# Performance work log

Hardware: AMD Instinct MI355X
Metric: run time of the kernel (lower is better)

## Reference

```python
import jax, jax.numpy as jnp
import numpy as np

D_MODEL = 512
D_INNER = 1024           # expand=2 * d_model
HEADDIM = 1024           # headdim = 2*hidden_dim -> nheads = 1
NHEADS = 1
D_STATE = 128            # Mamba2 default
D_CONV = 4               # Mamba2 default
CONV_DIM = D_INNER + 2 * D_STATE   # 1280
D_IN_PROJ = 2 * D_INNER + 2 * D_STATE + NHEADS  # 2305
BATCH, SEQ = 8, 2048
EPS = 1e-5


def setup_inputs() -> dict:
    key = jax.random.key(0)
    ks = jax.random.split(key, 8)
    x = jax.random.normal(ks[0], (BATCH, SEQ, D_MODEL), dtype=jnp.float32)
    rnn_state = jnp.zeros((1, BATCH, D_MODEL), dtype=jnp.float32)
    W_in = jax.random.normal(ks[1], (D_MODEL, D_IN_PROJ), dtype=jnp.float32) * 0.02
    conv_w = jax.random.normal(ks[2], (CONV_DIM, D_CONV), dtype=jnp.float32) * 0.2
    conv_b = jnp.zeros((CONV_DIM,), dtype=jnp.float32)
    dt_bias = jax.random.normal(ks[3], (NHEADS,), dtype=jnp.float32) * 0.1
    # A in (-16, -1): A_log = log(uniform(1,16))
    A_log = jnp.log(jax.random.uniform(ks[4], (NHEADS,), minval=1.0, maxval=16.0, dtype=jnp.float32))
    D = jnp.ones((NHEADS,), dtype=jnp.float32)
    norm_w = jnp.ones((D_INNER,), dtype=jnp.float32)
    W_out = jax.random.normal(ks[5], (D_INNER, D_MODEL), dtype=jnp.float32) * 0.02
    return {"x": x, "rnn_state": rnn_state, "W_in": W_in, "conv_w": conv_w,
            "conv_b": conv_b, "dt_bias": dt_bias, "A_log": A_log, "D": D,
            "norm_w": norm_w, "W_out": W_out}


def _mamba2_forward(x, W_in, conv_w, conv_b, dt_bias, A_log, D, norm_w, W_out):
    Bsz, T, _ = x.shape
    zxbcdt = x @ W_in                              # [B,T,2305]
    z = zxbcdt[..., :D_INNER]                      # [B,T,1024]
    xBC = zxbcdt[..., D_INNER:D_INNER + CONV_DIM]  # [B,T,1280]
    dt = zxbcdt[..., -NHEADS:]                     # [B,T,1]

    # causal depthwise conv1d over time, then silu
    xBC_t = jnp.transpose(xBC, (0, 2, 1))          # [B,C,T]
    w = conv_w[:, None, :]                          # [C,1,K]
    conv = jax.lax.conv_general_dilated(
        xBC_t, w, window_strides=(1,), padding=[(D_CONV - 1, 0)],
        feature_group_count=CONV_DIM, dimension_numbers=("NCH", "OIH", "NCH"))
    xBC = jax.nn.silu(jnp.transpose(conv, (0, 2, 1)) + conv_b)  # [B,T,1280]

    x_ssm = xBC[..., :D_INNER].reshape(Bsz, T, NHEADS, HEADDIM)  # [B,T,H,P]
    Bm = xBC[..., D_INNER:D_INNER + D_STATE]       # [B,T,N] (ngroups=1)
    Cm = xBC[..., -D_STATE:]                       # [B,T,N]

    dt = jax.nn.softplus(dt + dt_bias)             # [B,T,H]
    A = -jnp.exp(A_log)                            # [H]

    # selective SSM recurrence over time (time-major scan)
    xs = (jnp.transpose(x_ssm, (1, 0, 2, 3)),      # [T,B,H,P]
          jnp.transpose(dt, (1, 0, 2)),            # [T,B,H]
          jnp.transpose(Bm, (1, 0, 2)),            # [T,B,N]
          jnp.transpose(Cm, (1, 0, 2)))            # [T,B,N]
    h0 = jnp.zeros((Bsz, NHEADS, HEADDIM, D_STATE), dtype=x.dtype)

    def step(h, inp):
        xt, dtt, Bt, Ct = inp
        dA = jnp.exp(dtt * A)                      # [B,H]
        h = h * dA[:, :, None, None] + (dtt[:, :, None] * xt)[..., None] * Bt[:, None, None, :]
        y = jnp.einsum("bhpn,bn->bhp", h, Ct)
        return h, y

    _, ys = jax.lax.scan(step, h0, xs)             # ys: [T,B,H,P]
    y = jnp.transpose(ys, (1, 0, 2, 3)) + x_ssm * D[None, None, :, None]
    y = y.reshape(Bsz, T, D_INNER)

    # gated RMSNorm (norm_before_gate=False): rmsnorm(y * silu(z)) * weight
    y = y * jax.nn.silu(z)
    y = y * jax.lax.rsqrt(jnp.mean(y * y, axis=-1, keepdims=True) + EPS) * norm_w
    return y @ W_out                               # [B,T,D_MODEL]


def reference(x, rnn_state, W_in, conv_w, conv_b, dt_bias, A_log, D, norm_w, W_out):
    out = _mamba2_forward(x, W_in, conv_w, conv_b, dt_bias, A_log, D, norm_w, W_out)
    return (out, rnn_state)
```

## Files before the change

### kernel.cpp

```cpp
#include <hip/hip_runtime.h>
#include <hip/hip_bf16.h>
#include <math.h>

#define D_MODEL 512
#define D_INNER 1024
#define D_STATE 128
#define CONV_DIM (D_INNER + 2*D_STATE)
#define D_IN_PROJ (2*D_INNER + 2*D_STATE + 1)
#define NPROJ 2304
#define BATCH 8
#define SEQ 2048
#define NROWS (BATCH*SEQ)
#define CHUNK 128
#define NCHUNK (NROWS/CHUNK)
#define CPB (SEQ/CHUNK)
#define EPS_RMS 1e-5f

typedef __hip_bfloat16 bf16;
typedef __attribute__((ext_vector_type(8))) short short8;
typedef __attribute__((ext_vector_type(4))) float f32x4;

__device__ __forceinline__ float fbf(bf16 v) { return __bfloat162float(v); }
__device__ __forceinline__ bf16 tbf(float v) { return __float2bfloat16(v); }

__device__ __forceinline__ void gl2lds16(const bf16* g, bf16* l) {
    __builtin_amdgcn_global_load_lds(
        (const __attribute__((address_space(1))) unsigned int*)g,
        (__attribute__((address_space(3))) unsigned int*)l, 16, 0, 0);
}

__global__ void k_transpose_cvt(const float* __restrict__ src, bf16* __restrict__ dst,
                                int R, int C, int sstride) {
    __shared__ float tile[32][33];
    int c0 = blockIdx.x * 32, r0 = blockIdx.y * 32;
    int tx = threadIdx.x, ty = threadIdx.y;
    #pragma unroll
    for (int i = 0; i < 32; i += 8)
        tile[ty + i][tx] = src[(size_t)(c0 + ty + i) * sstride + (r0 + tx)];
    __syncthreads();
    #pragma unroll
    for (int i = 0; i < 32; i += 8)
        dst[(size_t)(r0 + ty + i) * C + (c0 + tx)] = tbf(tile[tx][ty + i]);
}

__global__ __launch_bounds__(256) void k_dtcvt(
    const float* __restrict__ x, const float* __restrict__ W_in,
    const float* __restrict__ dt_bias,
    bf16* __restrict__ xb, float* __restrict__ dts)
{
    __shared__ float wcol[D_MODEL];
    int tid = threadIdx.x;
    wcol[tid]       = W_in[(size_t)tid * D_IN_PROJ + 2304];
    wcol[tid + 256] = W_in[(size_t)(tid + 256) * D_IN_PROJ + 2304];
    __syncthreads();
    int row  = blockIdx.x * 4 + (tid >> 6);
    int lane = tid & 63;
    const float* xr = x + (size_t)row * D_MODEL;
    float4 a = *(const float4*)(xr + lane * 8);
    float4 b = *(const float4*)(xr + lane * 8 + 4);
    union { bf16 o[8]; uint4 u; } pk;
    pk.o[0]=tbf(a.x); pk.o[1]=tbf(a.y); pk.o[2]=tbf(a.z); pk.o[3]=tbf(a.w);
    pk.o[4]=tbf(b.x); pk.o[5]=tbf(b.y); pk.o[6]=tbf(b.z); pk.o[7]=tbf(b.w);
    *(uint4*)(xb + (size_t)row * D_MODEL + lane * 8) = pk.u;
    const float* wc = wcol + lane * 8;
    float s = a.x*wc[0]+a.y*wc[1]+a.z*wc[2]+a.w*wc[3]
            + b.x*wc[4]+b.y*wc[5]+b.z*wc[6]+b.w*wc[7];
    #pragma unroll
    for (int off = 32; off; off >>= 1) s += __shfl_xor(s, off);
    if (lane == 0) {
        float raw = s + dt_bias[0];
        dts[row] = raw > 20.f ? raw : log1pf(expf(raw));
    }
}

template<int MODE>
__global__ __launch_bounds__(256) void k_bgemm(
    const bf16* __restrict__ A, int lda, size_t sA,
    const bf16* __restrict__ Bt, int ldb, size_t sB,
    void* __restrict__ Cv, int ldc, size_t sC, int K)
{
    constexpr int BK = 64;
    __shared__ __align__(16) bf16 As[128][BK];
    __shared__ __align__(16) bf16 Bs[128][BK];
    const int tid = threadIdx.x, lane = tid & 63, wave = tid >> 6;
    const int wm = (wave & 1) * 64, wn = (wave >> 1) * 64;
    const int lr = lane & 15, quad = lane >> 4;
    const int rx = lr & 7;
    const size_t bm = (size_t)blockIdx.x * 128;
    const size_t bn = (size_t)blockIdx.y * 128;
    const size_t bi = blockIdx.z;
    A  += bi * sA;
    Bt += bi * sB;
    const int srow = lane >> 3;
    const int scol = (((lane & 7) ^ srow) << 3);

    f32x4 acc[4][4];
    #pragma unroll
    for (int i = 0; i < 4; ++i)
        #pragma unroll
        for (int j = 0; j < 4; ++j) acc[i][j] = (f32x4){0.f,0.f,0.f,0.f};

    for (int k0 = 0; k0 < K; k0 += BK) {
        __syncthreads();
        #pragma unroll
        for (int q = 0; q < 4; ++q) {
            int rg = wave * 32 + q * 8;
            gl2lds16(A  + (bm + rg + srow) * lda + k0 + scol, &As[rg][0]);
            gl2lds16(Bt + (bn + rg + srow) * ldb + k0 + scol, &Bs[rg][0]);
        }
        __syncthreads();
        #pragma unroll
        for (int ks = 0; ks < BK; ks += 32) {
            const int off = ((((ks >> 3) + quad) ^ rx) << 3);
            short8 af[4], bg[4];
            #pragma unroll
            for (int i = 0; i < 4; ++i)
                af[i] = *(const short8*)(&As[wm + i*16 + lr][off]);
            #pragma unroll
            for (int j = 0; j < 4; ++j)
                bg[j] = *(const short8*)(&Bs[wn + j*16 + lr][off]);
            #pragma unroll
            for (int i = 0; i < 4; ++i)
                #pragma unroll
                for (int j = 0; j < 4; ++j)
                    acc[i][j] = __builtin_amdgcn_mfma_f32_16x16x32_bf16(af[i], bg[j], acc[i][j], 0,0,0);
        }
    }
    #pragma unroll
    for (int i = 0; i < 4; ++i)
        #pragma unroll
        for (int j = 0; j < 4; ++j)
            #pragma unroll
            for (int r = 0; r < 4; ++r) {
                size_t row = bm + wm + i*16 + quad*4 + r;
                size_t col = bn + wn + j*16 + lr;
                float v = acc[i][j][r];
                if (MODE == 0) ((float*)Cv + bi*sC)[row * ldc + col] = v;
                else           ((bf16*)Cv + bi*sC)[row * ldc + col] = tbf(v);
            }
}

__global__ __launch_bounds__(256) void k_gemm_in(
    const bf16* __restrict__ A, const bf16* __restrict__ Bt,
    bf16* __restrict__ zb, bf16* __restrict__ xBCin, int K)
{
    constexpr int BK = 64;
    __shared__ __align__(16) bf16 As[128][BK];
    __shared__ __align__(16) bf16 Bs[128][BK];
    const int tid = threadIdx.x, lane = tid & 63, wave = tid >> 6;
    const int wm = (wave & 1) * 64, wn = (wave >> 1) * 64;
    const int lr = lane & 15, quad = lane >> 4;
    const int rx = lr & 7;
    const size_t bm = (size_t)blockIdx.x * 128;
    const int bn = blockIdx.y * 128;
    const int srow = lane >> 3;
    const int scol = (((lane & 7) ^ srow) << 3);

    f32x4 acc[4][4];
    #pragma unroll
    for (int i = 0; i < 4; ++i)
        #pragma unroll
        for (int j = 0; j < 4; ++j) acc[i][j] = (f32x4){0.f,0.f,0.f,0.f};

    for (int k0 = 0; k0 < K; k0 += BK) {
        __syncthreads();
        #pragma unroll
        for (int q = 0; q < 4; ++q) {
            int rg = wave * 32 + q * 8;
            gl2lds16(A  + (bm + rg + srow) * K + k0 + scol, &As[rg][0]);
            gl2lds16(Bt + ((size_t)bn + rg + srow) * K + k0 + scol, &Bs[rg][0]);
        }
        __syncthreads();
        #pragma unroll
        for (int ks = 0; ks < BK; ks += 32) {
            const int off = ((((ks >> 3) + quad) ^ rx) << 3);
            short8 af[4], bg[4];
            #pragma unroll
            for (int i = 0; i < 4; ++i)
                af[i] = *(const short8*)(&As[wm + i*16 + lr][off]);
            #pragma unroll
            for (int j = 0; j < 4; ++j)
                bg[j] = *(const short8*)(&Bs[wn + j*16 + lr][off]);
            #pragma unroll
            for (int i = 0; i < 4; ++i)
                #pragma unroll
                for (int j = 0; j < 4; ++j)
                    acc[i][j] = __builtin_amdgcn_mfma_f32_16x16x32_bf16(af[i], bg[j], acc[i][j], 0,0,0);
        }
    }
    #pragma unroll
    for (int i = 0; i < 4; ++i)
        #pragma unroll
        for (int j = 0; j < 4; ++j)
            #pragma unroll
            for (int r = 0; r < 4; ++r) {
                size_t row = bm + wm + i*16 + quad*4 + r;
                int col = bn + wn + j*16 + lr;
                float v = acc[i][j][r];
                if (col < D_INNER) zb[row * D_INNER + col] = tbf(v);
                else xBCin[row * CONV_DIM + (col - D_INNER)] = tbf(v);
            }
}

__global__ void k_prep(const float* __restrict__ dts, const float* __restrict__ A_log,
                       float* __restrict__ svec, float* __restrict__ wvec,
                       float* __restrict__ esvec, float* __restrict__ Pc)
{
    int chunk = blockIdx.x, t = threadIdx.x;
    int row = chunk * CHUNK + t;
    float A = -expf(A_log[0]);
    __shared__ float sh[CHUNK];
    sh[t] = A * dts[row];
    __syncthreads();
    for (int off = 1; off < CHUNK; off <<= 1) {
        float v = (t >= off) ? sh[t - off] : 0.f;
        __syncthreads();
        sh[t] += v;
        __syncthreads();
    }
    float s = sh[t], sL = sh[CHUNK - 1];
    svec[row]  = s;
    wvec[row]  = expf(sL - s) * dts[row];
    esvec[row] = expf(s);
    if (t == CHUNK - 1) Pc[chunk] = expf(sL);
}

__global__ __launch_bounds__(256) void k_ssd_bc(
    const bf16* __restrict__ xBCin, const float* __restrict__ conv_w,
    const float* __restrict__ conv_b, const float* __restrict__ wvec,
    const float* __restrict__ esvec, const float* __restrict__ svec,
    const float* __restrict__ dts, const float* __restrict__ Dp,
    bf16* __restrict__ Bw, bf16* __restrict__ A2)
{
    __shared__ __align__(16) bf16 Ls[131][128];
    __shared__ __align__(16) bf16 Bts[128][136];
    __shared__ __align__(16) bf16 Cts[128][136];
    __shared__ float sv_s[128], dt_s[128], wv_s[128], es_s[128];
    const int chunk = blockIdx.x;
    const int tid = threadIdx.x;
    const bool first = (chunk % CPB) == 0;
    const size_t rowbase = (size_t)chunk * CHUNK;
    if (tid < 128) {
        sv_s[tid] = svec[rowbase + tid];
        dt_s[tid] = dts[rowbase + tid];
        wv_s[tid] = wvec[rowbase + tid];
        es_s[tid] = esvec[rowbase + tid];
    }
    const int ch  = tid & 127;
    const int seg = tid >> 7;

    #pragma unroll
    for (int phase = 0; phase < 2; ++phase) {
        const int coff = D_INNER + phase * 128;
        __syncthreads();
        for (int i = tid; i < 131 * 16; i += 256) {
            int r = i >> 4, cg = (i & 15) << 3;
            uint4 v = (uint4){0,0,0,0};
            if (!(first && r < 3))
                v = *(const uint4*)(xBCin + (rowbase + r - 3) * CONV_DIM + coff + cg);
            *(uint4*)(&Ls[r][cg]) = v;
        }
        __syncthreads();
        float4 w = *(const float4*)(conv_w + (coff + ch) * 4);
        float bias = conv_b[coff + ch];
        float xv[11];
        #pragma unroll
        for (int i = 0; i < 3; ++i) xv[i + 8] = fbf(Ls[seg * 64 + i][ch]);
        for (int v = 0; v < 8; ++v) {
            int t0 = seg * 64 + v * 8;
            xv[0]=xv[8]; xv[1]=xv[9]; xv[2]=xv[10];
            #pragma unroll
            for (int i = 3; i < 11; ++i) xv[i] = fbf(Ls[t0 + i][ch]);
            float o[8];
            #pragma unroll
            for (int j = 0; j < 8; ++j) {
                float a = bias + w.x*xv[j] + w.y*xv[j+1] + w.z*xv[j+2] + w.w*xv[j+3];
                o[j] = a / (1.f + expf(-a));
            }
            if (phase == 0) {
                union { bf16 ob[8]; uint4 u; } pk;
                #pragma unroll
                for (int j = 0; j < 8; ++j) {
                    Bts[t0 + j][ch] = tbf(o[j]);
                    pk.ob[j] = tbf(o[j] * wv_s[t0 + j]);
                }
                *(uint4*)(Bw + (size_t)chunk*(D_STATE*CHUNK) + (size_t)ch*CHUNK + t0) = pk.u;
            } else {
                #pragma unroll
                for (int j = 0; j < 8; ++j) {
                    Cts[t0 + j][ch] = tbf(o[j]);
                    A2[(size_t)chunk*(CHUNK*256) + (size_t)(t0+j)*256 + 128 + ch] =
                        tbf(o[j] * es_s[t0 + j]);
                }
            }
        }
    }
    __syncthreads();
    const int lane = tid & 63, wave = tid >> 6;
    const int wm = (wave & 1) * 64, wn = (wave >> 1) * 64;
    const int lr = lane & 15, quad = lane >> 4;
    f32x4 acc[4][4];
    #pragma unroll
    for (int i = 0; i < 4; ++i)
        #pragma unroll
        for (int j = 0; j < 4; ++j) acc[i][j] = (f32x4){0.f,0.f,0.f,0.f};
    #pragma unroll
    for (int ks = 0; ks < 128; ks += 32) {
        short8 af[4], bg[4];
        #pragma unroll
        for (int i = 0; i < 4; ++i)
            af[i] = *(const short8*)(&Cts[wm + i*16 + lr][ks + quad*8]);
        #pragma unroll
        for (int j = 0; j < 4; ++j)
            bg[j] = *(const short8*)(&Bts[wn + j*16 + lr][ks + quad*8]);
        #pragma unroll
        for (int i = 0; i < 4; ++i)
            #pragma unroll
            for (int j = 0; j < 4; ++j)
                acc[i][j] = __builtin_amdgcn_mfma_f32_16x16x32_bf16(af[i], bg[j], acc[i][j], 0,0,0);
    }
    const float D0 = Dp[0];
    #pragma unroll
    for (int i = 0; i < 4; ++i)
        #pragma unroll
        for (int j = 0; j < 4; ++j)
            #pragma unroll
            for (int r = 0; r < 4; ++r) {
                int t = wm + i*16 + quad*4 + r;
                int u = wn + j*16 + lr;
                float o = 0.f;
                if (u <= t) {
                    o = acc[i][j][r] * expf(sv_s[t] - sv_s[u]) * dt_s[u];
                    if (u == t) o += D0;
                }
                A2[(size_t)chunk*(CHUNK*256) + (size_t)t*256 + u] = tbf(o);
            }
}

__global__ __launch_bounds__(256) void k_conv_xdh(
    const bf16* __restrict__ xBCin, const float* __restrict__ conv_w,
    const float* __restrict__ conv_b, const bf16* __restrict__ Bw,
    bf16* __restrict__ B2, bf16* __restrict__ dH)
{
    __shared__ __align__(16) bf16 Ls[131][128];
    __shared__ __align__(16) bf16 Xs[128][136];
    __shared__ __align__(16) bf16 Bws[128][136];
    const int chunk = blockIdx.y;
    const int p0 = blockIdx.x * 128;
    const int tid = threadIdx.x;
    const bool first = (chunk % CPB) == 0;
    const size_t rowbase = (size_t)chunk * CHUNK;
    for (int i = tid; i < 131 * 16; i += 256) {
        int r = i >> 4, cg = (i & 15) << 3;
        uint4 v = (uint4){0,0,0,0};
        if (!(first && r < 3))
            v = *(const uint4*)(xBCin + (rowbase + r - 3) * CONV_DIM + p0 + cg);
        *(uint4*)(&Ls[r][cg]) = v;
    }
    for (int i = tid; i < 128 * 16; i += 256) {
        int nr = i >> 4, cg = (i & 15) << 3;
        *(uint4*)(&Bws[nr][cg]) =
            *(const uint4*)(Bw + (size_t)chunk*(D_STATE*CHUNK) + (size_t)nr*CHUNK + cg);
    }
    __syncthreads();
    const int p = tid & 127;
    const int half = tid >> 7;
    const int ch = p0 + p;
    float4 w = *(const float4*)(conv_w + ch * 4);
    float bias = conv_b[ch];
    bf16* outrow = B2 + (size_t)chunk * (D_INNER * 256) + (size_t)ch * 256;
    float xv[11];
    #pragma unroll
    for (int i = 0; i < 3; ++i) xv[i + 8] = fbf(Ls[half * 64 + i][p]);
    for (int v = 0; v < 8; ++v) {
        int t0 = half * 64 + v * 8;
        xv[0]=xv[8]; xv[1]=xv[9]; xv[2]=xv[10];
        #pragma unroll
        for (int i = 3; i < 11; ++i) xv[i] = fbf(Ls[t0 + i][p]);
        union { bf16 o[8]; uint4 u; } pk;
        #pragma unroll
        for (int j = 0; j < 8; ++j) {
            float a = bias + w.x*xv[j] + w.y*xv[j+1] + w.z*xv[j+2] + w.w*xv[j+3];
            pk.o[j] = tbf(a / (1.f + expf(-a)));
        }
        *(uint4*)(outrow + t0) = pk.u;
        *(uint4*)(&Xs[p][t0]) = pk.u;
    }
    __syncthreads();
    const int lane = tid & 63, wave = tid >> 6;
    const int wm = (wave & 1) * 64, wn = (wave >> 1) * 64;
    const int lr = lane & 15, quad = lane >> 4;
    f32x4 acc[4][4];
    #pragma unroll
    for (int i = 0; i < 4; ++i)
        #pragma unroll
        for (int j = 0; j < 4; ++j) acc[i][j] = (f32x4){0.f,0.f,0.f,0.f};
    #pragma unroll
    for (int ks = 0; ks < 128; ks += 32) {
        short8 af[4], bg[4];
        #pragma unroll
        for (int i = 0; i < 4; ++i)
            af[i] = *(const short8*)(&Xs[wm + i*16 + lr][ks + quad*8]);
        #pragma unroll
        for (int j = 0; j < 4; ++j)
            bg[j] = *(const short8*)(&Bws[wn + j*16 + lr][ks + quad*8]);
        #pragma unroll
        for (int i = 0; i < 4; ++i)
            #pragma unroll
            for (int j = 0; j < 4; ++j)
                acc[i][j] = __builtin_amdgcn_mfma_f32_16x16x32_bf16(af[i], bg[j], acc[i][j], 0,0,0);
    }
    #pragma unroll
    for (int i = 0; i < 4; ++i)
        #pragma unroll
        for (int j = 0; j < 4; ++j)
            #pragma unroll
            for (int r = 0; r < 4; ++r) {
                int pr = p0 + wm + i*16 + quad*4 + r;
                int n  = wn + j*16 + lr;
                dH[(size_t)chunk*(D_INNER*D_STATE) + (size_t)pr*D_STATE + n] = tbf(acc[i][j][r]);
            }
}

__global__ void k_carry(const bf16* __restrict__ dH, const float* __restrict__ Pc,
                        bf16* __restrict__ B2)
{
    int idx = blockIdx.x * 256 + threadIdx.x;
    int b = blockIdx.y;
    int p = idx >> 7, n = idx & 127;
    float v[CPB], pc[CPB];
    #pragma unroll
    for (int c = 0; c < CPB; ++c)
        v[c] = fbf(dH[(size_t)(b*CPB + c) * (D_INNER*D_STATE) + idx]);
    #pragma unroll
    for (int c = 0; c < CPB; ++c) pc[c] = Pc[b*CPB + c];
    float h = 0.f;
    #pragma unroll
    for (int c = 0; c < CPB; ++c) {
        int bi = b * CPB + c;
        B2[(size_t)bi * (D_INNER*256) + (size_t)p * 256 + 128 + n] = tbf(h);
        h = pc[c] * h + v[c];
    }
}

__global__ __launch_bounds__(256) void k_gate_norm(
    bf16* __restrict__ y, const bf16* __restrict__ zb,
    const float* __restrict__ norm_w)
{
    int row  = blockIdx.x * 4 + (threadIdx.x >> 6);
    int lane = threadIdx.x & 63;
    bf16* yr = y + (size_t)row * D_INNER;
    const bf16* zr = zb + (size_t)row * D_INNER;
    const int c0 = lane * 8, c1 = 512 + lane * 8;
    union { bf16 b[8]; uint4 u; } y0, y1, z0, z1;
    y0.u = *(const uint4*)(yr + c0); y1.u = *(const uint4*)(yr + c1);
    z0.u = *(const uint4*)(zr + c0); z1.u = *(const uint4*)(zr + c1);
    float v[16], ss = 0.f;
    #pragma unroll
    for (int j = 0; j < 8; ++j) {
        float z = fbf(z0.b[j]);
        v[j] = fbf(y0.b[j]) * z / (1.f + expf(-z));
        ss += v[j] * v[j];
    }
    #pragma unroll
    for (int j = 0; j < 8; ++j) {
        float z = fbf(z1.b[j]);
        v[8+j] = fbf(y1.b[j]) * z / (1.f + expf(-z));
        ss += v[8+j] * v[8+j];
    }
    #pragma unroll
    for (int off = 32; off; off >>= 1) ss += __shfl_xor(ss, off);
    float scale = rsqrtf(ss * (1.f / D_INNER) + EPS_RMS);
    union { bf16 b[8]; uint4 u; } p0, p1;
    #pragma unroll
    for (int j = 0; j < 8; ++j) p0.b[j] = tbf(v[j]   * scale * norm_w[c0 + j]);
    #pragma unroll
    for (int j = 0; j < 8; ++j) p1.b[j] = tbf(v[8+j] * scale * norm_w[c1 + j]);
    *(uint4*)(yr + c0) = p0.u;
    *(uint4*)(yr + c1) = p1.u;
}

extern "C" void kernel_launch(void* const* d_in, const int* in_sizes, int n_in,
                              void* d_out, int out_size, void* d_ws, size_t ws_size,
                              hipStream_t stream)
{
    const float* x       = (const float*)d_in[0];
    const float* rnn     = (const float*)d_in[1];
    const float* W_in    = (const float*)d_in[2];
    const float* conv_w  = (const float*)d_in[3];
    const float* conv_b  = (const float*)d_in[4];
    const float* dt_bias = (const float*)d_in[5];
    const float* A_log   = (const float*)d_in[6];
    const float* Dp      = (const float*)d_in[7];
    const float* norm_w  = (const float*)d_in[8];
    const float* W_out   = (const float*)d_in[9];
    float* out = (float*)d_out;

    char* ws = (char*)d_ws;
    size_t off = 0;
    auto alloc = [&](size_t bytes) { void* p = ws + off; off += (bytes + 255) & ~255ULL; return p; };

    bf16*  W_inbT  = (bf16*) alloc((size_t)NPROJ * D_MODEL * 2);
    bf16*  W_outbT = (bf16*) alloc((size_t)D_MODEL * D_INNER * 2);
    float* dts     = (float*)alloc((size_t)NROWS * 4);
    float* svec    = (float*)alloc((size_t)NROWS * 4);
    float* wvec    = (float*)alloc((size_t)NROWS * 4);
    float* esvec   = (float*)alloc((size_t)NROWS * 4);
    float* Pc      = (float*)alloc((size_t)NCHUNK * 4);
    bf16*  zb      = (bf16*) alloc((size_t)NROWS * D_INNER * 2);
    bf16*  A2      = (bf16*) alloc((size_t)NCHUNK * CHUNK * 256 * 2);
    bf16*  B2      = (bf16*) alloc((size_t)NCHUNK * D_INNER * 256 * 2);
    bf16*  Bw      = (bf16*) alloc((size_t)NCHUNK * D_STATE * CHUNK * 2);
    char* RA = (char*)alloc((size_t)NROWS * D_MODEL * 2 + (size_t)NROWS * D_INNER * 2);
    bf16*  xb   = (bf16*)RA;
    bf16*  dH   = (bf16*)(RA + (size_t)NROWS * D_MODEL * 2);
    bf16*  ybf  = (bf16*)RA;
    bf16*  xBCin = (bf16*)alloc((size_t)NROWS * CONV_DIM * 2);

    k_dtcvt<<<NROWS / 4, 256, 0, stream>>>(x, W_in, dt_bias, xb, dts);
    k_transpose_cvt<<<dim3(D_MODEL/32, NPROJ/32), dim3(32, 8), 0, stream>>>(
        W_in, W_inbT, NPROJ, D_MODEL, D_IN_PROJ);
    k_transpose_cvt<<<dim3(D_INNER/32, D_MODEL/32), dim3(32, 8), 0, stream>>>(
        W_out, W_outbT, D_MODEL, D_INNER, D_MODEL);
    k_prep<<<NCHUNK, CHUNK, 0, stream>>>(dts, A_log, svec, wvec, esvec, Pc);

    k_gemm_in<<<dim3(NROWS/128, NPROJ/128), 256, 0, stream>>>(xb, W_inbT, zb, xBCin, D_MODEL);

    k_ssd_bc<<<NCHUNK, 256, 0, stream>>>(xBCin, conv_w, conv_b, wvec, esvec,
                                         svec, dts, Dp, Bw, A2);

    k_conv_xdh<<<dim3(8, NCHUNK), 256, 0, stream>>>(xBCin, conv_w, conv_b, Bw, B2, dH);

    k_carry<<<dim3(D_INNER*D_STATE/256, BATCH), 256, 0, stream>>>(dH, Pc, B2);

    k_bgemm<1><<<dim3(1, D_INNER/128, NCHUNK), 256, 0, stream>>>(
        A2, 256, (size_t)CHUNK*256,
        B2, 256, (size_t)D_INNER*256,
        ybf, D_INNER, (size_t)CHUNK*D_INNER, 256);

    k_gate_norm<<<NROWS / 4, 256, 0, stream>>>(ybf, zb, norm_w);

    k_bgemm<0><<<dim3(NROWS/128, D_MODEL/128, 1), 256, 0, stream>>>(
        ybf, D_INNER, 0, W_outbT, D_INNER, 0, out, D_MODEL, 0, D_INNER);

    hipMemcpyAsync(out + (size_t)NROWS * D_MODEL, rnn,
                   (size_t)BATCH * D_MODEL * sizeof(float),
                   hipMemcpyDeviceToDevice, stream);
}
```

Measured before the change: 323.1 us.

## Fuse gated RMSNorm into SSD output and out-projection GEMM epilogues

```diff
diff --git a/kernel.cpp b/kernel.cpp
--- a/kernel.cpp
+++ b/kernel.cpp
@@ -30,13 +30,15 @@
 }
 
 __global__ void k_transpose_cvt(const float* __restrict__ src, bf16* __restrict__ dst,
-                                int R, int C, int sstride) {
+                                int R, int C, int sstride, const float* __restrict__ scale) {
     __shared__ float tile[32][33];
     int c0 = blockIdx.x * 32, r0 = blockIdx.y * 32;
     int tx = threadIdx.x, ty = threadIdx.y;
     #pragma unroll
-    for (int i = 0; i < 32; i += 8)
-        tile[ty + i][tx] = src[(size_t)(c0 + ty + i) * sstride + (r0 + tx)];
+    for (int i = 0; i < 32; i += 8) {
+        float s = scale ? scale[c0 + ty + i] : 1.f;
+        tile[ty + i][tx] = src[(size_t)(c0 + ty + i) * sstride + (r0 + tx)] * s;
+    }
     __syncthreads();
     #pragma unroll
     for (int i = 0; i < 32; i += 8)
@@ -77,7 +79,8 @@
 __global__ __launch_bounds__(256) void k_bgemm(
     const bf16* __restrict__ A, int lda, size_t sA,
     const bf16* __restrict__ Bt, int ldb, size_t sB,
-    void* __restrict__ Cv, int ldc, size_t sC, int K)
+    void* __restrict__ Cv, int ldc, size_t sC, int K,
+    const bf16* __restrict__ zg, float* __restrict__ ssq)
 {
     constexpr int BK = 64;
     __shared__ __align__(16) bf16 As[128][BK];
@@ -126,18 +129,65 @@
                     acc[i][j] = __builtin_amdgcn_mfma_f32_16x16x32_bf16(af[i], bg[j], acc[i][j], 0,0,0);
         }
     }
-    #pragma unroll
-    for (int i = 0; i < 4; ++i)
-        #pragma unroll
-        for (int j = 0; j < 4; ++j)
+    if (MODE <= 1) {
+        #pragma unroll
+        for (int i = 0; i < 4; ++i)
+            #pragma unroll
+            for (int j = 0; j < 4; ++j)
+                #pragma unroll
+                for (int r = 0; r < 4; ++r) {
+                    size_t row = bm + wm + i*16 + quad*4 + r;
+                    size_t col = bn + wn + j*16 + lr;
+                    float v = acc[i][j][r];
+                    if (MODE == 0) ((float*)Cv + bi*sC)[row * ldc + col] = v;
+                    else           ((bf16*)Cv + bi*sC)[row * ldc + col] = tbf(v);
+                }
+    } else if (MODE == 2) {
+        const size_t tokbase = bi * CHUNK;
+        float srw[4][4];
+        #pragma unroll
+        for (int i = 0; i < 4; ++i)
+            #pragma unroll
+            for (int r = 0; r < 4; ++r) srw[i][r] = 0.f;
+        #pragma unroll
+        for (int i = 0; i < 4; ++i)
+            #pragma unroll
+            for (int j = 0; j < 4; ++j)
+                #pragma unroll
+                for (int r = 0; r < 4; ++r) {
+                    size_t row = bm + wm + i*16 + quad*4 + r;
+                    size_t col = bn + wn + j*16 + lr;
+                    float z = fbf(zg[(tokbase + row) * D_INNER + col]);
+                    float g = acc[i][j][r] * z / (1.f + expf(-z));
+                    ((bf16*)Cv + bi*sC)[row * ldc + col] = tbf(g);
+                    srw[i][r] += g * g;
+                }
+        #pragma unroll
+        for (int i = 0; i < 4; ++i)
+            #pragma unroll
+            for (int r = 0; r < 4; ++r) {
+                float s = srw[i][r];
+                s += __shfl_xor(s, 1);
+                s += __shfl_xor(s, 2);
+                s += __shfl_xor(s, 4);
+                s += __shfl_xor(s, 8);
+                if (lr == 0)
+                    atomicAdd(ssq + tokbase + bm + wm + i*16 + quad*4 + r, s);
+            }
+    } else {
+        #pragma unroll
+        for (int i = 0; i < 4; ++i)
             #pragma unroll
             for (int r = 0; r < 4; ++r) {
                 size_t row = bm + wm + i*16 + quad*4 + r;
-                size_t col = bn + wn + j*16 + lr;
-                float v = acc[i][j][r];
-                if (MODE == 0) ((float*)Cv + bi*sC)[row * ldc + col] = v;
-                else           ((bf16*)Cv + bi*sC)[row * ldc + col] = tbf(v);
-            }
+                float sc = rsqrtf(ssq[row] * (1.f / D_INNER) + EPS_RMS);
+                #pragma unroll
+                for (int j = 0; j < 4; ++j) {
+                    size_t col = bn + wn + j*16 + lr;
+                    ((float*)Cv + bi*sC)[row * ldc + col] = acc[i][j][r] * sc;
+                }
+            }
+    }
 }
 
 __global__ __launch_bounds__(256) void k_gemm_in(
@@ -344,7 +394,6 @@
 {
     __shared__ __align__(16) bf16 Ls[131][128];
     __shared__ __align__(16) bf16 Xs[128][136];
-    __shared__ __align__(16) bf16 Bws[128][136];
     const int chunk = blockIdx.y;
     const int p0 = blockIdx.x * 128;
     const int tid = threadIdx.x;
@@ -357,11 +406,6 @@
             v = *(const uint4*)(xBCin + (rowbase + r - 3) * CONV_DIM + p0 + cg);
         *(uint4*)(&Ls[r][cg]) = v;
     }
-    for (int i = tid; i < 128 * 16; i += 256) {
-        int nr = i >> 4, cg = (i & 15) << 3;
-        *(uint4*)(&Bws[nr][cg]) =
-            *(const uint4*)(Bw + (size_t)chunk*(D_STATE*CHUNK) + (size_t)nr*CHUNK + cg);
-    }
     __syncthreads();
     const int p = tid & 127;
     const int half = tid >> 7;
@@ -390,6 +434,7 @@
     const int lane = tid & 63, wave = tid >> 6;
     const int wm = (wave & 1) * 64, wn = (wave >> 1) * 64;
     const int lr = lane & 15, quad = lane >> 4;
+    const bf16* bwc = Bw + (size_t)chunk * (D_STATE * CHUNK);
     f32x4 acc[4][4];
     #pragma unroll
     for (int i = 0; i < 4; ++i)
@@ -399,11 +444,11 @@
     for (int ks = 0; ks < 128; ks += 32) {
         short8 af[4], bg[4];
         #pragma unroll
+        for (int j = 0; j < 4; ++j)
+            bg[j] = *(const short8*)(bwc + (size_t)(wn + j*16 + lr) * CHUNK + ks + quad*8);
+        #pragma unroll
         for (int i = 0; i < 4; ++i)
             af[i] = *(const short8*)(&Xs[wm + i*16 + lr][ks + quad*8]);
-        #pragma unroll
-        for (int j = 0; j < 4; ++j)
-            bg[j] = *(const short8*)(&Bws[wn + j*16 + lr][ks + quad*8]);
         #pragma unroll
         for (int i = 0; i < 4; ++i)
             #pragma unroll
@@ -422,62 +467,30 @@
             }
 }
 
-__global__ void k_carry(const bf16* __restrict__ dH, const float* __restrict__ Pc,
-                        bf16* __restrict__ B2)
+__global__ __launch_bounds__(256) void k_carry(
+    const bf16* __restrict__ dH, const float* __restrict__ Pc, bf16* __restrict__ B2)
 {
     int idx = blockIdx.x * 256 + threadIdx.x;
     int b = blockIdx.y;
-    int p = idx >> 7, n = idx & 127;
-    float v[CPB], pc[CPB];
+    int p = idx >> 4, ng = (idx & 15) << 3;
+    uint4 v[CPB];
+    float pc[CPB];
     #pragma unroll
     for (int c = 0; c < CPB; ++c)
-        v[c] = fbf(dH[(size_t)(b*CPB + c) * (D_INNER*D_STATE) + idx]);
+        v[c] = *(const uint4*)(dH + (size_t)(b*CPB + c)*(D_INNER*D_STATE) + (size_t)p*D_STATE + ng);
     #pragma unroll
     for (int c = 0; c < CPB; ++c) pc[c] = Pc[b*CPB + c];
-    float h = 0.f;
+    float h[8] = {0,0,0,0,0,0,0,0};
     #pragma unroll
     for (int c = 0; c < CPB; ++c) {
-        int bi = b * CPB + c;
-        B2[(size_t)bi * (D_INNER*256) + (size_t)p * 256 + 128 + n] = tbf(h);
-        h = pc[c] * h + v[c];
-    }
-}
-
-__global__ __launch_bounds__(256) void k_gate_norm(
-    bf16* __restrict__ y, const bf16* __restrict__ zb,
-    const float* __restrict__ norm_w)
-{
-    int row  = blockIdx.x * 4 + (threadIdx.x >> 6);
-    int lane = threadIdx.x & 63;
-    bf16* yr = y + (size_t)row * D_INNER;
-    const bf16* zr = zb + (size_t)row * D_INNER;
-    const int c0 = lane * 8, c1 = 512 + lane * 8;
-    union { bf16 b[8]; uint4 u; } y0, y1, z0, z1;
-    y0.u = *(const uint4*)(yr + c0); y1.u = *(const uint4*)(yr + c1);
-    z0.u = *(const uint4*)(zr + c0); z1.u = *(const uint4*)(zr + c1);
-    float v[16], ss = 0.f;
-    #pragma unroll
-    for (int j = 0; j < 8; ++j) {
-        float z = fbf(z0.b[j]);
-        v[j] = fbf(y0.b[j]) * z / (1.f + expf(-z));
-        ss += v[j] * v[j];
-    }
-    #pragma unroll
-    for (int j = 0; j < 8; ++j) {
-        float z = fbf(z1.b[j]);
-        v[8+j] = fbf(y1.b[j]) * z / (1.f + expf(-z));
-        ss += v[8+j] * v[8+j];
-    }
-    #pragma unroll
-    for (int off = 32; off; off >>= 1) ss += __shfl_xor(ss, off);
-    float scale = rsqrtf(ss * (1.f / D_INNER) + EPS_RMS);
-    union { bf16 b[8]; uint4 u; } p0, p1;
-    #pragma unroll
-    for (int j = 0; j < 8; ++j) p0.b[j] = tbf(v[j]   * scale * norm_w[c0 + j]);
-    #pragma unroll
-    for (int j = 0; j < 8; ++j) p1.b[j] = tbf(v[8+j] * scale * norm_w[c1 + j]);
-    *(uint4*)(yr + c0) = p0.u;
-    *(uint4*)(yr + c1) = p1.u;
+        union { bf16 o[8]; uint4 u; } pk;
+        #pragma unroll
+        for (int k = 0; k < 8; ++k) pk.o[k] = tbf(h[k]);
+        *(uint4*)(B2 + (size_t)(b*CPB + c)*(D_INNER*256) + (size_t)p*256 + 128 + ng) = pk.u;
+        const bf16* vb = (const bf16*)&v[c];
+        #pragma unroll
+        for (int k = 0; k < 8; ++k) h[k] = pc[c]*h[k] + fbf(vb[k]);
+    }
 }
 
 extern "C" void kernel_launch(void* const* d_in, const int* in_sizes, int n_in,
@@ -507,6 +520,7 @@
     float* wvec    = (float*)alloc((size_t)NROWS * 4);
     float* esvec   = (float*)alloc((size_t)NROWS * 4);
     float* Pc      = (float*)alloc((size_t)NCHUNK * 4);
+    float* ssq     = (float*)alloc((size_t)NROWS * 4);
     bf16*  zb      = (bf16*) alloc((size_t)NROWS * D_INNER * 2);
     bf16*  A2      = (bf16*) alloc((size_t)NCHUNK * CHUNK * 256 * 2);
     bf16*  B2      = (bf16*) alloc((size_t)NCHUNK * D_INNER * 256 * 2);
@@ -517,11 +531,13 @@
     bf16*  ybf  = (bf16*)RA;
     bf16*  xBCin = (bf16*)alloc((size_t)NROWS * CONV_DIM * 2);
 
+    hipMemsetAsync(ssq, 0, (size_t)NROWS * sizeof(float), stream);
+
     k_dtcvt<<<NROWS / 4, 256, 0, stream>>>(x, W_in, dt_bias, xb, dts);
     k_transpose_cvt<<<dim3(D_MODEL/32, NPROJ/32), dim3(32, 8), 0, stream>>>(
-        W_in, W_inbT, NPROJ, D_MODEL, D_IN_PROJ);
+        W_in, W_inbT, NPROJ, D_MODEL, D_IN_PROJ, nullptr);
     k_transpose_cvt<<<dim3(D_INNER/32, D_MODEL/32), dim3(32, 8), 0, stream>>>(
-        W_out, W_outbT, D_MODEL, D_INNER, D_MODEL);
+        W_out, W_outbT, D_MODEL, D_INNER, D_MODEL, norm_w);
     k_prep<<<NCHUNK, CHUNK, 0, stream>>>(dts, A_log, svec, wvec, esvec, Pc);
 
     k_gemm_in<<<dim3(NROWS/128, NPROJ/128), 256, 0, stream>>>(xb, W_inbT, zb, xBCin, D_MODEL);
@@ -531,17 +547,16 @@
 
     k_conv_xdh<<<dim3(8, NCHUNK), 256, 0, stream>>>(xBCin, conv_w, conv_b, Bw, B2, dH);
 
-    k_carry<<<dim3(D_INNER*D_STATE/256, BATCH), 256, 0, stream>>>(dH, Pc, B2);
-
-    k_bgemm<1><<<dim3(1, D_INNER/128, NCHUNK), 256, 0, stream>>>(
+    k_carry<<<dim3(64, BATCH), 256, 0, stream>>>(dH, Pc, B2);
+
+    k_bgemm<2><<<dim3(1, D_INNER/128, NCHUNK), 256, 0, stream>>>(
         A2, 256, (size_t)CHUNK*256,
         B2, 256, (size_t)D_INNER*256,
-        ybf, D_INNER, (size_t)CHUNK*D_INNER, 256);
-
-    k_gate_norm<<<NROWS / 4, 256, 0, stream>>>(ybf, zb, norm_w);
-
-    k_bgemm<0><<<dim3(NROWS/128, D_MODEL/128, 1), 256, 0, stream>>>(
-        ybf, D_INNER, 0, W_outbT, D_INNER, 0, out, D_MODEL, 0, D_INNER);
+        ybf, D_INNER, (size_t)CHUNK*D_INNER, 256, zb, ssq);
+
+    k_bgemm<3><<<dim3(NROWS/128, D_MODEL/128, 1), 256, 0, stream>>>(
+        ybf, D_INNER, 0, W_outbT, D_INNER, 0, out, D_MODEL, 0, D_INNER,
+        nullptr, ssq);
 
     hipMemcpyAsync(out + (size_t)NROWS * D_MODEL, rnn,
                    (size_t)BATCH * D_MODEL * sizeof(float),
```

Measured after the change: 321.1 us. Within noise of the previous version (-0.6%).
